# Performance work log

Hardware: AMD Instinct MI355X
Metric: run time of the kernel (lower is better)

Reference implementation:

```python
import jax, jax.numpy as jnp
import numpy as np

B, N, D, H = 8, 128, 768, 64
NEG = -1e30
SLOPE = 0.01  # LeakyReLU slope
EPS = 1e-5    # BatchNorm eps


def setup_inputs() -> dict:
    key = jax.random.key(0)
    ks = jax.random.split(key, 10)
    s = 0.02
    feature = jax.random.normal(ks[0], (B, N, D), jnp.float32)
    aspect = jax.random.normal(ks[1], (B, D), jnp.float32)
    adj = jax.random.randint(ks[2], (B, N, N), 0, 2).astype(jnp.int32)
    W0 = jax.random.normal(ks[3], (D, D), jnp.float32) * s
    b0 = jnp.zeros((D,), jnp.float32)
    W1 = jax.random.normal(ks[4], (D, D), jnp.float32) * s
    b1 = jnp.zeros((D,), jnp.float32)
    A1 = jax.random.normal(ks[5], (2 * D, H), jnp.float32) * s  # afcs[0]
    ab1 = jnp.zeros((H,), jnp.float32)
    A2 = jax.random.normal(ks[6], (H, 1), jnp.float32) * s      # afcs[2]
    ab2 = jnp.zeros((1,), jnp.float32)
    gamma = jnp.ones((D,), jnp.float32)
    beta = jnp.zeros((D,), jnp.float32)
    return dict(feature=feature, aspect=aspect, adj=adj, W0=W0, b0=b0,
                W1=W1, b1=b1, A1=A1, ab1=ab1, A2=A2, ab2=ab2,
                gamma=gamma, beta=beta)


def reference(feature, aspect, adj, W0, b0, W1, b1, A1, ab1, A2, ab2, gamma, beta):
    # aspect is unused by the original forward.
    m = adj.astype(feature.dtype)          # [B,N,N] 0/1 mask
    d = A1.shape[0] // 2
    A1s, A1t = A1[:d], A1[d:]              # weight-split of Linear(2*mem_dim, H):
                                           # [h_i, h_j] @ A1 == h_i @ A1s + h_j @ A1t
    for (W, b) in ((W0, b0), (W1, b1)):
        h = feature @ W + b                # [B,N,D]
        s_src = h @ A1s                    # [B,N,H], broadcast over j
        s_tgt = h @ A1t                    # [B,N,H], broadcast over i
        hid = jax.nn.relu(s_src[:, :, None, :] + s_tgt[:, None, :, :] + ab1)  # [B,N,N,H]
        e = (hid @ A2)[..., 0] + ab2[0]    # [B,N,N]
        e = jnp.where(e > 0, e, SLOPE * e)  # LeakyReLU(0.01)
        logits = e * m + (1.0 - m) * NEG    # mask_logits
        b_, n_ = logits.shape[0], logits.shape[1]
        # NOTE: original softmaxes over the FLATTENED N*N axis, not per-row.
        attn = jax.nn.softmax(logits.reshape(b_, n_ * n_), axis=-1).reshape(b_, n_, n_)
        feature = jnp.einsum('bij,bjd->bid', attn, h)  # attention.bmm(h)
        # dropout is identity in eval / deterministic reference
    node_feature = feature
    g = node_feature.sum(axis=1)           # [B,D]
    mean = g.mean(axis=0)
    var = g.var(axis=0)                    # biased, matches BN training forward
    graph_feature = gamma * (g - mean) / jnp.sqrt(var + EPS) + beta
    return graph_feature, node_feature
```

## Files before the change

kernel.cpp:

```cpp
#include <hip/hip_runtime.h>
#include <math.h>

#define NEG_V (-1e30f)
#define SLOPE_V 0.01f
#define EPS_V 1e-5f

typedef __attribute__((ext_vector_type(8))) short bs8;
typedef __attribute__((ext_vector_type(4))) float f32x4;

__device__ __forceinline__ void split2(float x, unsigned short& hi, unsigned short& lo) {
    unsigned u = __float_as_uint(x);
    unsigned h = (u + 0x7FFFu + ((u >> 16) & 1u)) >> 16;
    hi = (unsigned short)h;
    float hf = __uint_as_float(h << 16);
    float l = x - hf;
    unsigned ul = __float_as_uint(l);
    lo = (unsigned short)((ul + 0x7FFFu + ((ul >> 16) & 1u)) >> 16);
}

__device__ __forceinline__ void mfma_loop(
    const unsigned short* __restrict__ Ahg, const unsigned short* __restrict__ Alg,
    int lda,
    const unsigned short* __restrict__ Bhg, const unsigned short* __restrict__ Blg,
    int ldb, int K, int row0, int col0,
    f32x4 (&acc)[2][2],
    unsigned short (*Ah)[40], unsigned short (*Al)[40],
    unsigned short (*Bh)[40], unsigned short (*Bl)[40])
{
    const int tid = threadIdx.x;
    const int lane = tid & 63, wid = tid >> 6;
    const int wm0 = (wid >> 1) * 32, wn0 = (wid & 1) * 32;
    const int lm = lane & 15, q = lane >> 4;
    const int sr = tid >> 2, sc = (tid & 3) * 8;

    for (int k0 = 0; k0 < K; k0 += 32) {
        *(bs8*)&Ah[sr][sc] = *(const bs8*)(Ahg + (size_t)(row0 + sr) * lda + k0 + sc);
        *(bs8*)&Al[sr][sc] = *(const bs8*)(Alg + (size_t)(row0 + sr) * lda + k0 + sc);
        *(bs8*)&Bh[sr][sc] = *(const bs8*)(Bhg + (size_t)(col0 + sr) * ldb + k0 + sc);
        *(bs8*)&Bl[sr][sc] = *(const bs8*)(Blg + (size_t)(col0 + sr) * ldb + k0 + sc);
        __syncthreads();

        bs8 a_h[2], a_l[2], b_h[2], b_l[2];
#pragma unroll
        for (int t = 0; t < 2; t++) {
            a_h[t] = *(bs8*)&Ah[wm0 + t * 16 + lm][q * 8];
            a_l[t] = *(bs8*)&Al[wm0 + t * 16 + lm][q * 8];
            b_h[t] = *(bs8*)&Bh[wn0 + t * 16 + lm][q * 8];
            b_l[t] = *(bs8*)&Bl[wn0 + t * 16 + lm][q * 8];
        }
#pragma unroll
        for (int mt = 0; mt < 2; mt++)
#pragma unroll
            for (int nt = 0; nt < 2; nt++) {
                acc[mt][nt] = __builtin_amdgcn_mfma_f32_16x16x32_bf16(a_h[mt], b_h[nt], acc[mt][nt], 0, 0, 0);
                acc[mt][nt] = __builtin_amdgcn_mfma_f32_16x16x32_bf16(a_h[mt], b_l[nt], acc[mt][nt], 0, 0, 0);
                acc[mt][nt] = __builtin_amdgcn_mfma_f32_16x16x32_bf16(a_l[mt], b_h[nt], acc[mt][nt], 0, 0, 0);
            }
        __syncthreads();
    }
}

__device__ __forceinline__ void transpose_split_tile(
    const float* __restrict__ src, int src_ld,
    unsigned short* __restrict__ dh, unsigned short* __restrict__ dl, int dst_ld,
    unsigned short (*Th)[72], unsigned short (*Tl)[72])
{
    int tid = threadIdx.x;
    int r = tid >> 2;
    int cb = (tid & 3) * 16;
#pragma unroll
    for (int cc = 0; cc < 16; cc += 4) {
        float4 v = *(const float4*)(src + (size_t)r * src_ld + cb + cc);
        unsigned short hh, ll;
        split2(v.x, hh, ll); Th[cb + cc + 0][r] = hh; Tl[cb + cc + 0][r] = ll;
        split2(v.y, hh, ll); Th[cb + cc + 1][r] = hh; Tl[cb + cc + 1][r] = ll;
        split2(v.z, hh, ll); Th[cb + cc + 2][r] = hh; Tl[cb + cc + 2][r] = ll;
        split2(v.w, hh, ll); Th[cb + cc + 3][r] = hh; Tl[cb + cc + 3][r] = ll;
    }
    __syncthreads();
    int n = tid >> 2, ch = (tid & 3) * 8;
    *(bs8*)(dh + (size_t)n * dst_ld + ch)      = *(bs8*)&Th[n][ch];
    *(bs8*)(dh + (size_t)n * dst_ld + ch + 32) = *(bs8*)&Th[n][ch + 32];
    *(bs8*)(dl + (size_t)n * dst_ld + ch)      = *(bs8*)&Tl[n][ch];
    *(bs8*)(dl + (size_t)n * dst_ld + ch + 32) = *(bs8*)&Tl[n][ch + 32];
}

__device__ __forceinline__ void flat_split_job(
    const float* __restrict__ src, unsigned short* __restrict__ dh,
    unsigned short* __restrict__ dl, size_t base)
{
    unsigned short hh, ll;
#pragma unroll
    for (int g = 0; g < 2; g++) {
        bs8 sh, sl;
#pragma unroll
        for (int cc = 0; cc < 8; cc += 4) {
            float4 v = *(const float4*)(src + base + g * 8 + cc);
            split2(v.x, hh, ll); sh[cc + 0] = (short)hh; sl[cc + 0] = (short)ll;
            split2(v.y, hh, ll); sh[cc + 1] = (short)hh; sl[cc + 1] = (short)ll;
            split2(v.z, hh, ll); sh[cc + 2] = (short)hh; sl[cc + 2] = (short)ll;
            split2(v.w, hh, ll); sh[cc + 3] = (short)hh; sl[cc + 3] = (short)ll;
        }
        *(bs8*)(dh + base + g * 8) = sh;
        *(bs8*)(dl + base + g * 8) = sl;
    }
}

__global__ __launch_bounds__(256) void prep_k(
    const float* __restrict__ W0, const float* __restrict__ W1,
    const float* __restrict__ A1, const float* __restrict__ feature,
    const float* __restrict__ b0, const float* __restrict__ b1,
    unsigned short* Wt0h, unsigned short* Wt0l,
    unsigned short* Wt1h, unsigned short* Wt1l,
    unsigned short* fh, unsigned short* fl,
    unsigned short* WAth, unsigned short* WAtl,
    float* bA)
{
    __shared__ __align__(16) char smem[20480];
    int id = blockIdx.x, tid = threadIdx.x;
    if (id < 288) {
        unsigned short (*Th)[72] = (unsigned short(*)[72])(smem);
        unsigned short (*Tl)[72] = (unsigned short(*)[72])(smem + 9216);
        if (id < 144) {
            int kt = id / 12, nt = id % 12;
            transpose_split_tile(W0 + (size_t)(kt * 64) * 768 + nt * 64, 768,
                                 Wt0h + (size_t)(nt * 64) * 768 + kt * 64,
                                 Wt0l + (size_t)(nt * 64) * 768 + kt * 64, 768, Th, Tl);
        } else {
            int r = id - 144, kt = r / 12, nt = r % 12;
            transpose_split_tile(W1 + (size_t)(kt * 64) * 768 + nt * 64, 768,
                                 Wt1h + (size_t)(nt * 64) * 768 + kt * 64,
                                 Wt1l + (size_t)(nt * 64) * 768 + kt * 64, 768, Th, Tl);
        }
    } else if (id < 480) {
        flat_split_job(feature, fh, fl, (size_t)(id - 288) * 4096 + tid * 16);
    } else if (id < 528) {
        int j = id - 480;
        int rt = j % 12, ct = (j / 12) & 1, layer = j / 24;
        const float* W = layer ? W1 : W0;
        const int r0 = rt * 64;
        unsigned short (*Ah)[40] = (unsigned short(*)[40])(smem);
        unsigned short (*Al)[40] = (unsigned short(*)[40])(smem + 5120);
        unsigned short (*Bh)[40] = (unsigned short(*)[40])(smem + 10240);
        unsigned short (*Bl)[40] = (unsigned short(*)[40])(smem + 15360);
        const int lane = tid & 63, wid = tid >> 6;
        const int wm0 = (wid >> 1) * 32, wn0 = (wid & 1) * 32;
        const int lm = lane & 15, q = lane >> 4;
        const int akk = tid & 31, acs = (tid >> 5) * 8;
        const int br = tid >> 2, bks = (tid & 3) * 8;
        f32x4 acc[2][2] = {};
        for (int k0 = 0; k0 < 768; k0 += 32) {
            {
                const float* ap = A1 + (size_t)(ct * 768 + k0 + akk) * 64 + acs;
                float4 v0 = *(const float4*)ap;
                float4 v1 = *(const float4*)(ap + 4);
                unsigned short hv, lv;
                split2(v0.x, hv, lv); Ah[acs + 0][akk] = hv; Al[acs + 0][akk] = lv;
                split2(v0.y, hv, lv); Ah[acs + 1][akk] = hv; Al[acs + 1][akk] = lv;
                split2(v0.z, hv, lv); Ah[acs + 2][akk] = hv; Al[acs + 2][akk] = lv;
                split2(v0.w, hv, lv); Ah[acs + 3][akk] = hv; Al[acs + 3][akk] = lv;
                split2(v1.x, hv, lv); Ah[acs + 4][akk] = hv; Al[acs + 4][akk] = lv;
                split2(v1.y, hv, lv); Ah[acs + 5][akk] = hv; Al[acs + 5][akk] = lv;
                split2(v1.z, hv, lv); Ah[acs + 6][akk] = hv; Al[acs + 6][akk] = lv;
                split2(v1.w, hv, lv); Ah[acs + 7][akk] = hv; Al[acs + 7][akk] = lv;
            }
            {
                const float* wp = W + (size_t)(r0 + br) * 768 + k0 + bks;
                float4 v0 = *(const float4*)wp;
                float4 v1 = *(const float4*)(wp + 4);
                bs8 sh, sl; unsigned short hv, lv;
                split2(v0.x, hv, lv); sh[0] = (short)hv; sl[0] = (short)lv;
                split2(v0.y, hv, lv); sh[1] = (short)hv; sl[1] = (short)lv;
                split2(v0.z, hv, lv); sh[2] = (short)hv; sl[2] = (short)lv;
                split2(v0.w, hv, lv); sh[3] = (short)hv; sl[3] = (short)lv;
                split2(v1.x, hv, lv); sh[4] = (short)hv; sl[4] = (short)lv;
                split2(v1.y, hv, lv); sh[5] = (short)hv; sl[5] = (short)lv;
                split2(v1.z, hv, lv); sh[6] = (short)hv; sl[6] = (short)lv;
                split2(v1.w, hv, lv); sh[7] = (short)hv; sl[7] = (short)lv;
                *(bs8*)&Bh[br][bks] = sh;
                *(bs8*)&Bl[br][bks] = sl;
            }
            __syncthreads();
            bs8 a_h[2], a_l[2], b_h[2], b_l[2];
#pragma unroll
            for (int t = 0; t < 2; t++) {
                a_h[t] = *(bs8*)&Ah[wm0 + t * 16 + lm][q * 8];
                a_l[t] = *(bs8*)&Al[wm0 + t * 16 + lm][q * 8];
                b_h[t] = *(bs8*)&Bh[wn0 + t * 16 + lm][q * 8];
                b_l[t] = *(bs8*)&Bl[wn0 + t * 16 + lm][q * 8];
            }
#pragma unroll
            for (int mt = 0; mt < 2; mt++)
#pragma unroll
                for (int nt = 0; nt < 2; nt++) {
                    acc[mt][nt] = __builtin_amdgcn_mfma_f32_16x16x32_bf16(a_h[mt], b_h[nt], acc[mt][nt], 0, 0, 0);
                    acc[mt][nt] = __builtin_amdgcn_mfma_f32_16x16x32_bf16(a_h[mt], b_l[nt], acc[mt][nt], 0, 0, 0);
                    acc[mt][nt] = __builtin_amdgcn_mfma_f32_16x16x32_bf16(a_l[mt], b_h[nt], acc[mt][nt], 0, 0, 0);
                }
            __syncthreads();
        }
        const int c0 = ct * 64;
        size_t base = (size_t)layer * 98304;
#pragma unroll
        for (int mt = 0; mt < 2; mt++)
#pragma unroll
            for (int nt = 0; nt < 2; nt++) {
                int n = r0 + wn0 + nt * 16 + lm;
#pragma unroll
                for (int i = 0; i < 4; i++) {
                    int m = c0 + wm0 + mt * 16 + q * 4 + i;
                    unsigned short hv, lv;
                    split2(acc[mt][nt][i], hv, lv);
                    WAth[base + (size_t)m * 768 + n] = hv;
                    WAtl[base + (size_t)m * 768 + n] = lv;
                }
            }
    } else {
        float* redb = (float*)(smem);
        int layer = id - 528;
        const float* bv = layer ? b1 : b0;
        int c = tid & 127, half = tid >> 7;
        float acc = 0.f;
        for (int kk = 0; kk < 384; kk++) {
            int k = half * 384 + kk;
            int row = (c < 64 ? k : 768 + k);
            acc += bv[k] * A1[(size_t)row * 64 + (c & 63)];
        }
        redb[tid] = acc;
        __syncthreads();
        if (tid < 128) bA[layer * 128 + tid] = redb[tid] + redb[tid + 128];
    }
}

__global__ __launch_bounds__(256) void gemm_fused_k(
    const unsigned short* __restrict__ Ahg, const unsigned short* __restrict__ Alg,
    const unsigned short* __restrict__ Wth, const unsigned short* __restrict__ Wtl,
    const unsigned short* __restrict__ WAth, const unsigned short* __restrict__ WAtl,
    const float* __restrict__ bias,
    unsigned short* __restrict__ hth, unsigned short* __restrict__ htl,
    float* __restrict__ s)
{
    __shared__ unsigned short smem[4][64][40];
    int bx = blockIdx.x, row0 = blockIdx.y * 64;
    const unsigned short* Bh;
    const unsigned short* Bl;
    int col0;
    if (bx < 12) { Bh = Wth;  Bl = Wtl;  col0 = bx * 64; }
    else         { Bh = WAth; Bl = WAtl; col0 = (bx - 12) * 64; }
    f32x4 acc[2][2] = {};
    mfma_loop(Ahg, Alg, 768, Bh, Bl, 768, 768, row0, col0, acc,
              smem[0], smem[1], smem[2], smem[3]);
    int tid = threadIdx.x, lane = tid & 63, wid = tid >> 6;
    int wm0 = (wid >> 1) * 32, wn0 = (wid & 1) * 32;
    int lm = lane & 15, q = lane >> 4;
    if (bx >= 12) {
#pragma unroll
        for (int mt = 0; mt < 2; mt++)
#pragma unroll
            for (int nt = 0; nt < 2; nt++) {
                int c = col0 + wn0 + nt * 16 + lm;
#pragma unroll
                for (int i = 0; i < 4; i++) {
                    int r = row0 + wm0 + mt * 16 + q * 4 + i;
                    s[(size_t)r * 128 + c] = acc[mt][nt][i];
                }
            }
        return;
    }
    __syncthreads();
    unsigned short* flat = &smem[0][0][0];
    unsigned short (*Hi)[69] = (unsigned short(*)[69])flat;
    unsigned short (*Lo)[69] = (unsigned short(*)[69])(flat + 4416);
#pragma unroll
    for (int mt = 0; mt < 2; mt++)
#pragma unroll
        for (int nt = 0; nt < 2; nt++) {
            int c = wn0 + nt * 16 + lm;
            float bv = bias[col0 + c];
#pragma unroll
            for (int i = 0; i < 4; i++) {
                int r = wm0 + mt * 16 + q * 4 + i;
                unsigned short hv, lv;
                split2(acc[mt][nt][i] + bv, hv, lv);
                Hi[r][c] = hv; Lo[r][c] = lv;
            }
        }
    __syncthreads();
    int d = tid >> 2, kq = (tid & 3) * 16;
    int b = row0 >> 7, kb = row0 & 127;
    bs8 th0, th1, tl0, tl1;
#pragma unroll
    for (int e = 0; e < 8; e++) {
        th0[e] = Hi[kq + e][d];     th1[e] = Hi[kq + 8 + e][d];
        tl0[e] = Lo[kq + e][d];     tl1[e] = Lo[kq + 8 + e][d];
    }
    size_t to = ((size_t)b * 768 + col0 + d) * 128 + kb + kq;
    *(bs8*)(hth + to) = th0; *(bs8*)(hth + to + 8) = th1;
    *(bs8*)(htl + to) = tl0; *(bs8*)(htl + to + 8) = tl1;
}

__global__ __launch_bounds__(256) void score_k(
    const float* __restrict__ s, const int* __restrict__ adj,
    const float* __restrict__ ab1, const float* __restrict__ A2,
    const float* __restrict__ ab2, const float* __restrict__ bA,
    unsigned short* __restrict__ ph, unsigned short* __restrict__ pl,
    float* __restrict__ psum)
{
    __shared__ float st[128][65];
    __shared__ float ss[4][65];
    __shared__ float a2s[64];
    __shared__ float warr[4];
    const int bx = blockIdx.x, b = blockIdx.y, tid = threadIdx.x;
    const int i0 = bx * 4;
    for (int idx = tid; idx < 8192; idx += 256) {
        int j = idx >> 6, h2 = idx & 63;
        st[j][h2] = s[(size_t)(b * 128 + j) * 128 + 64 + h2] + bA[64 + h2];
    }
    {
        int i = tid >> 6, h2 = tid & 63;
        ss[i][h2] = s[(size_t)(b * 128 + i0 + i) * 128 + h2] + bA[h2] + ab1[h2];
    }
    if (tid < 64) a2s[tid] = A2[tid];
    __syncthreads();
    const float ab2v = ab2[0];
    const int rr = tid >> 7;
    const int j = tid & 127;
    const int r0 = rr * 2, r1 = rr * 2 + 1;
    float acc0 = 0.f, acc1 = 0.f;
#pragma unroll 4
    for (int h2 = 0; h2 < 64; h2++) {
        float bb = st[j][h2];
        float cv = a2s[h2];
        acc0 = fmaf(fmaxf(ss[r0][h2] + bb, 0.f), cv, acc0);
        acc1 = fmaf(fmaxf(ss[r1][h2] + bb, 0.f), cv, acc1);
    }
    float e0 = acc0 + ab2v; e0 = (e0 > 0.f) ? e0 : SLOPE_V * e0;
    float e1 = acc1 + ab2v; e1 = (e1 > 0.f) ? e1 : SLOPE_V * e1;
    size_t o0 = (size_t)b * 16384 + (size_t)(i0 + r0) * 128 + j;
    size_t o1 = (size_t)b * 16384 + (size_t)(i0 + r1) * 128 + j;
    float v0 = adj[o0] ? expf(e0) : 0.f;
    float v1 = adj[o1] ? expf(e1) : 0.f;
    unsigned short hv, lv;
    split2(v0, hv, lv); ph[o0] = hv; pl[o0] = lv;
    split2(v1, hv, lv); ph[o1] = hv; pl[o1] = lv;
    float vs = v0 + v1;
#pragma unroll
    for (int o = 32; o > 0; o >>= 1) vs += __shfl_down(vs, o);
    if ((tid & 63) == 0) warr[tid >> 6] = vs;
    __syncthreads();
    if (tid == 0) psum[b * 32 + bx] = warr[0] + warr[1] + warr[2] + warr[3];
}

__global__ __launch_bounds__(256) void attn_mfma_k(
    const unsigned short* __restrict__ ph, const unsigned short* __restrict__ pl,
    const unsigned short* __restrict__ hth, const unsigned short* __restrict__ htl,
    const float* __restrict__ psum, float* __restrict__ node,
    unsigned short* __restrict__ nodeh, unsigned short* __restrict__ nodel)
{
    __shared__ unsigned short smem[4][64][40];
    __shared__ float sred[33];
    int b = blockIdx.z;
    int row0 = blockIdx.y * 64, col0 = blockIdx.x * 64;
    int tid = threadIdx.x;
    if (tid < 32) sred[tid] = psum[b * 32 + tid];
    __syncthreads();
    if (tid == 0) {
        float t = 0.f;
#pragma unroll
        for (int i = 0; i < 32; i++) t += sred[i];
        sred[32] = 1.0f / t;
    }
    __syncthreads();
    float alpha = sred[32];
    f32x4 acc[2][2] = {};
    mfma_loop(ph + (size_t)b * 16384, pl + (size_t)b * 16384, 128,
              hth + (size_t)b * 98304, htl + (size_t)b * 98304, 128, 128,
              row0, col0, acc, smem[0], smem[1], smem[2], smem[3]);
    __syncthreads();
    float* C = node + (size_t)b * 98304;
    unsigned short* flat = &smem[0][0][0];
    unsigned short (*Hi)[69] = (unsigned short(*)[69])flat;
    unsigned short (*Lo)[69] = (unsigned short(*)[69])(flat + 4416);
    int lane = tid & 63, wid = tid >> 6;
    int wm0 = (wid >> 1) * 32, wn0 = (wid & 1) * 32;
    int lm = lane & 15, q = lane >> 4;
#pragma unroll
    for (int mt = 0; mt < 2; mt++)
#pragma unroll
        for (int nt = 0; nt < 2; nt++) {
            int c = wn0 + nt * 16 + lm;
#pragma unroll
            for (int i = 0; i < 4; i++) {
                int r = wm0 + mt * 16 + q * 4 + i;
                float v = acc[mt][nt][i] * alpha;
                C[(size_t)(row0 + r) * 768 + col0 + c] = v;
                unsigned short hv, lv;
                split2(v, hv, lv);
                Hi[r][c] = hv; Lo[r][c] = lv;
            }
        }
    __syncthreads();
    int r = tid >> 2, cq = (tid & 3) * 16;
    bs8 vh0, vh1, vl0, vl1;
#pragma unroll
    for (int e = 0; e < 8; e++) {
        vh0[e] = Hi[r][cq + e];     vh1[e] = Hi[r][cq + 8 + e];
        vl0[e] = Lo[r][cq + e];     vl1[e] = Lo[r][cq + 8 + e];
    }
    size_t ro = (size_t)(b * 128 + row0 + r) * 768 + col0 + cq;
    *(bs8*)(nodeh + ro) = vh0; *(bs8*)(nodeh + ro + 8) = vh1;
    *(bs8*)(nodel + ro) = vl0; *(bs8*)(nodel + ro + 8) = vl1;
}

__global__ __launch_bounds__(512) void gsum_bnorm_k(
    const float* __restrict__ node, const float* __restrict__ gamma,
    const float* __restrict__ beta, float* __restrict__ out)
{
    __shared__ float gbuf[8][64];
    __shared__ float mean_s[64], inv_s[64];
    int tid = threadIdx.x;
    int bg = tid >> 6, dl = tid & 63;
    int d = blockIdx.x * 64 + dl;
    float v = 0.f;
    for (int i = 0; i < 128; i++)
        v += node[(size_t)(bg * 128 + i) * 768 + d];
    gbuf[bg][dl] = v;
    __syncthreads();
    if (tid < 64) {
        float m = 0.f;
#pragma unroll
        for (int b = 0; b < 8; b++) m += gbuf[b][tid];
        m *= 0.125f;
        float var = 0.f;
#pragma unroll
        for (int b = 0; b < 8; b++) { float t = gbuf[b][tid] - m; var += t * t; }
        var *= 0.125f;
        mean_s[tid] = m;
        inv_s[tid] = 1.0f / sqrtf(var + EPS_V);
    }
    __syncthreads();
    out[bg * 768 + d] = gamma[d] * (v - mean_s[dl]) * inv_s[dl] + beta[d];
}

extern "C" void kernel_launch(void* const* d_in, const int* in_sizes, int n_in,
                              void* d_out, int out_size, void* d_ws, size_t ws_size,
                              hipStream_t stream)
{
    const float* feature = (const float*)d_in[0];
    const int*   adj     = (const int*)d_in[2];
    const float* W0      = (const float*)d_in[3];
    const float* b0      = (const float*)d_in[4];
    const float* W1      = (const float*)d_in[5];
    const float* b1      = (const float*)d_in[6];
    const float* A1      = (const float*)d_in[7];
    const float* ab1     = (const float*)d_in[8];
    const float* A2      = (const float*)d_in[9];
    const float* ab2     = (const float*)d_in[10];
    const float* gamma   = (const float*)d_in[11];
    const float* beta    = (const float*)d_in[12];

    float* ws    = (float*)d_ws;
    float* s     = ws;
    float* psum  = ws + 131072;
    float* bA    = ws + 131328;
    unsigned short* u = (unsigned short*)(ws + 131584);
    unsigned short* Wt0h = u;
    unsigned short* Wt0l = Wt0h + 589824;
    unsigned short* Wt1h = Wt0l + 589824;
    unsigned short* Wt1l = Wt1h + 589824;
    unsigned short* WAth = Wt1l + 589824;
    unsigned short* WAtl = WAth + 196608;
    unsigned short* fh   = WAtl + 196608;
    unsigned short* fl   = fh + 786432;
    unsigned short* hth  = fl + 786432;
    unsigned short* htl  = hth + 786432;
    unsigned short* ndh  = htl + 786432;
    unsigned short* ndl  = ndh + 786432;
    unsigned short* ph   = ndl + 786432;
    unsigned short* pl   = ph + 131072;

    float* out       = (float*)d_out;
    float* graph_out = out;
    float* node_out  = out + 6144;

    prep_k<<<530, 256, 0, stream>>>(W0, W1, A1, feature, b0, b1,
                                    Wt0h, Wt0l, Wt1h, Wt1l,
                                    fh, fl, WAth, WAtl, bA);

    for (int layer = 0; layer < 2; layer++) {
        const unsigned short* Wth = layer ? Wt1h : Wt0h;
        const unsigned short* Wtl = layer ? Wt1l : Wt0l;
        const float* bb = layer ? b1 : b0;
        const unsigned short* Ahg = layer ? ndh : fh;
        const unsigned short* Alg = layer ? ndl : fl;
        gemm_fused_k<<<dim3(14, 16), 256, 0, stream>>>(
            Ahg, Alg, Wth, Wtl, WAth + (size_t)layer * 98304,
            WAtl + (size_t)layer * 98304, bb, hth, htl, s);
        score_k<<<dim3(32, 8), 256, 0, stream>>>(s, adj, ab1, A2, ab2,
                                                 bA + layer * 128, ph, pl, psum);
        attn_mfma_k<<<dim3(12, 2, 8), 256, 0, stream>>>(ph, pl, hth, htl, psum,
                                                        node_out, ndh, ndl);
    }
    gsum_bnorm_k<<<12, 512, 0, stream>>>(node_out, gamma, beta, graph_out);
}
```

Before: 181.6 us.

## Double-buffer shared tiles and prefetch next K-slice into registers in MFMA loop

```diff
diff --git a/kernel.cpp b/kernel.cpp
--- a/kernel.cpp
+++ b/kernel.cpp
@@ -24,8 +24,7 @@
     const unsigned short* __restrict__ Bhg, const unsigned short* __restrict__ Blg,
     int ldb, int K, int row0, int col0,
     f32x4 (&acc)[2][2],
-    unsigned short (*Ah)[40], unsigned short (*Al)[40],
-    unsigned short (*Bh)[40], unsigned short (*Bl)[40])
+    unsigned short (*buf)[64][40])
 {
     const int tid = threadIdx.x;
     const int lane = tid & 63, wid = tid >> 6;
@@ -33,13 +32,33 @@
     const int lm = lane & 15, q = lane >> 4;
     const int sr = tid >> 2, sc = (tid & 3) * 8;
 
+    const unsigned short* pAh = Ahg + (size_t)(row0 + sr) * lda + sc;
+    const unsigned short* pAl = Alg + (size_t)(row0 + sr) * lda + sc;
+    const unsigned short* pBh = Bhg + (size_t)(col0 + sr) * ldb + sc;
+    const unsigned short* pBl = Blg + (size_t)(col0 + sr) * ldb + sc;
+
+    bs8 rAh = *(const bs8*)(pAh);
+    bs8 rAl = *(const bs8*)(pAl);
+    bs8 rBh = *(const bs8*)(pBh);
+    bs8 rBl = *(const bs8*)(pBl);
+
+    int st = 0;
     for (int k0 = 0; k0 < K; k0 += 32) {
-        *(bs8*)&Ah[sr][sc] = *(const bs8*)(Ahg + (size_t)(row0 + sr) * lda + k0 + sc);
-        *(bs8*)&Al[sr][sc] = *(const bs8*)(Alg + (size_t)(row0 + sr) * lda + k0 + sc);
-        *(bs8*)&Bh[sr][sc] = *(const bs8*)(Bhg + (size_t)(col0 + sr) * ldb + k0 + sc);
-        *(bs8*)&Bl[sr][sc] = *(const bs8*)(Blg + (size_t)(col0 + sr) * ldb + k0 + sc);
+        unsigned short (*Ah)[40] = buf[st * 4 + 0];
+        unsigned short (*Al)[40] = buf[st * 4 + 1];
+        unsigned short (*Bh)[40] = buf[st * 4 + 2];
+        unsigned short (*Bl)[40] = buf[st * 4 + 3];
+        *(bs8*)&Ah[sr][sc] = rAh;
+        *(bs8*)&Al[sr][sc] = rAl;
+        *(bs8*)&Bh[sr][sc] = rBh;
+        *(bs8*)&Bl[sr][sc] = rBl;
         __syncthreads();
-
+        if (k0 + 32 < K) {
+            rAh = *(const bs8*)(pAh + k0 + 32);
+            rAl = *(const bs8*)(pAl + k0 + 32);
+            rBh = *(const bs8*)(pBh + k0 + 32);
+            rBl = *(const bs8*)(pBl + k0 + 32);
+        }
         bs8 a_h[2], a_l[2], b_h[2], b_l[2];
 #pragma unroll
         for (int t = 0; t < 2; t++) {
@@ -56,7 +75,7 @@
                 acc[mt][nt] = __builtin_amdgcn_mfma_f32_16x16x32_bf16(a_h[mt], b_l[nt], acc[mt][nt], 0, 0, 0);
                 acc[mt][nt] = __builtin_amdgcn_mfma_f32_16x16x32_bf16(a_l[mt], b_h[nt], acc[mt][nt], 0, 0, 0);
             }
-        __syncthreads();
+        st ^= 1;
     }
 }
 
@@ -240,7 +259,7 @@
     unsigned short* __restrict__ hth, unsigned short* __restrict__ htl,
     float* __restrict__ s)
 {
-    __shared__ unsigned short smem[4][64][40];
+    __shared__ unsigned short smem[8][64][40];
     int bx = blockIdx.x, row0 = blockIdx.y * 64;
     const unsigned short* Bh;
     const unsigned short* Bl;
@@ -248,8 +267,7 @@
     if (bx < 12) { Bh = Wth;  Bl = Wtl;  col0 = bx * 64; }
     else         { Bh = WAth; Bl = WAtl; col0 = (bx - 12) * 64; }
     f32x4 acc[2][2] = {};
-    mfma_loop(Ahg, Alg, 768, Bh, Bl, 768, 768, row0, col0, acc,
-              smem[0], smem[1], smem[2], smem[3]);
+    mfma_loop(Ahg, Alg, 768, Bh, Bl, 768, 768, row0, col0, acc, smem);
     int tid = threadIdx.x, lane = tid & 63, wid = tid >> 6;
     int wm0 = (wid >> 1) * 32, wn0 = (wid & 1) * 32;
     int lm = lane & 15, q = lane >> 4;
@@ -357,7 +375,7 @@
     const float* __restrict__ psum, float* __restrict__ node,
     unsigned short* __restrict__ nodeh, unsigned short* __restrict__ nodel)
 {
-    __shared__ unsigned short smem[4][64][40];
+    __shared__ unsigned short smem[8][64][40];
     __shared__ float sred[33];
     int b = blockIdx.z;
     int row0 = blockIdx.y * 64, col0 = blockIdx.x * 64;
@@ -375,7 +393,7 @@
     f32x4 acc[2][2] = {};
     mfma_loop(ph + (size_t)b * 16384, pl + (size_t)b * 16384, 128,
               hth + (size_t)b * 98304, htl + (size_t)b * 98304, 128, 128,
-              row0, col0, acc, smem[0], smem[1], smem[2], smem[3]);
+              row0, col0, acc, smem);
     __syncthreads();
     float* C = node + (size_t)b * 98304;
     unsigned short* flat = &smem[0][0][0];
```

Result: faster. 176.7 us (-2.7%).
